# Performance work log

Hardware: AMD Instinct MI355X
Metric: run time of the kernel (lower is better)

The kernel has to match this reference:

```python
import jax, jax.numpy as jnp
import numpy as np

D_MODEL = 256
D_HID = 128
EPS = 1e-5
MASK_VALUE = -10000.0


def _layer_norm(x, scale, bias):
    mu = jnp.mean(x, axis=-1, keepdims=True)
    var = jnp.mean(jnp.square(x - mu), axis=-1, keepdims=True)
    return (x - mu) * jax.lax.rsqrt(var + EPS) * scale + bias


def setup_inputs() -> dict:
    key = jax.random.key(0)
    ks = jax.random.split(key, 8)
    B, S = 32, 1024
    std = 0.02
    return {
        "x": jax.random.normal(ks[0], (B, S, D_MODEL), dtype=jnp.float32),
        "ln1_scale": jnp.ones((D_MODEL,), jnp.float32),
        "ln1_bias": jnp.zeros((D_MODEL,), jnp.float32),
        "w_qkv": jax.random.normal(ks[1], (D_MODEL, 3 * D_MODEL), jnp.float32) * std,
        "b_qkv": jnp.zeros((3 * D_MODEL,), jnp.float32),
        "w_proj": jax.random.normal(ks[2], (D_MODEL, D_MODEL), jnp.float32) * std,
        "b_proj": jnp.zeros((D_MODEL,), jnp.float32),
        "ln2_scale": jnp.ones((D_MODEL,), jnp.float32),
        "ln2_bias": jnp.zeros((D_MODEL,), jnp.float32),
        "w_fc1": jax.random.normal(ks[3], (D_MODEL, D_HID), jnp.float32) * std,
        "b_fc1": jnp.zeros((D_HID,), jnp.float32),
        "w_fc2": jax.random.normal(ks[4], (D_HID, D_MODEL), jnp.float32) * std,
        "b_fc2": jnp.zeros((D_MODEL,), jnp.float32),
    }


def reference(x, ln1_scale, ln1_bias, w_qkv, b_qkv, w_proj, b_proj,
              ln2_scale, ln2_bias, w_fc1, b_fc1, w_fc2, b_fc2):
    B, S, D = x.shape
    # --- pre-LN self-attention ---
    residual = x
    h = _layer_norm(x, ln1_scale, ln1_bias)
    qkv = h @ w_qkv + b_qkv                       # [B, S, 3D]
    q, k, v = jnp.split(qkv, 3, axis=2)           # each [B, S, D]; 1 head, head_dim=D
    scale = 1.0 / jnp.sqrt(jnp.asarray(D, x.dtype))
    scores = jnp.einsum('bqd,bkd->bqk', q, k) * scale   # [B, S, S]
    causal = jnp.tril(jnp.ones((S, S), dtype=bool))
    scores = jnp.where(causal[None, :, :], scores, MASK_VALUE)
    attn = jax.nn.softmax(scores, axis=-1)        # dropout is identity (eval mode)
    out = jnp.einsum('bqk,bkd->bqd', attn, v)     # [B, S, D]
    out = out @ w_proj + b_proj
    x = out + residual
    # --- pre-LN MLP ---
    residual = x
    h = _layer_norm(x, ln2_scale, ln2_bias)
    h = jax.nn.relu(h @ w_fc1 + b_fc1)
    h = h @ w_fc2 + b_fc2
    return h + residual
```

## Files before the change

### kernel.cpp

```cpp
#include <hip/hip_runtime.h>
#include <hip/hip_bf16.h>

#define D_MODEL 256
#define D_HID   128
#define SEQ     1024
#define NBATCH  32
#define NROWS   (NBATCH * SEQ)
#define MASKV   -10000.0f
#define EPSLN   1e-5f

typedef unsigned short u16;
using bf16x8 = __attribute__((ext_vector_type(8))) short;
using f32x4  = __attribute__((ext_vector_type(4))) float;

union U8 { uint4 v; u16 s[8]; };

__device__ __forceinline__ float bf2f(u16 u) {
    unsigned int x = ((unsigned int)u) << 16;
    return __uint_as_float(x);
}
__device__ __forceinline__ u16 f2bf(float f) {
    unsigned int u = __float_as_uint(f);
    u += 0x7fff + ((u >> 16) & 1);
    return (u16)(u >> 16);
}
__device__ __forceinline__ void load4(const float* p, float* f) {
    float4 a = *(const float4*)p;
    f[0] = a.x; f[1] = a.y; f[2] = a.z; f[3] = a.w;
}
__device__ __forceinline__ void load4(const u16* p, float* f) {
    ushort4 v = *(const ushort4*)p;
    f[0] = bf2f(v.x); f[1] = bf2f(v.y); f[2] = bf2f(v.z); f[3] = bf2f(v.w);
}
__device__ __forceinline__ void gload16(const u16* g, u16* l) {
    __builtin_amdgcn_global_load_lds(
        (const __attribute__((address_space(1))) void*)g,
        (__attribute__((address_space(3))) void*)l, 16, 0, 0);
}

template <int CTRL>
__device__ __forceinline__ float dpp_mov(float v) {
    return __int_as_float(__builtin_amdgcn_update_dpp(
        0, __float_as_int(v), CTRL, 0xf, 0xf, true));
}
__device__ __forceinline__ float red16_max(float v) {
    v = fmaxf(v, dpp_mov<0xB1>(v));
    v = fmaxf(v, dpp_mov<0x4E>(v));
    v = fmaxf(v, dpp_mov<0x141>(v));
    v = fmaxf(v, dpp_mov<0x140>(v));
    return v;
}
__device__ __forceinline__ float red16_sum(float v) {
    v += dpp_mov<0xB1>(v);
    v += dpp_mov<0x4E>(v);
    v += dpp_mov<0x141>(v);
    v += dpp_mov<0x140>(v);
    return v;
}

__global__ __launch_bounds__(256) void transpose_weights(
    const float* __restrict__ wqkv, u16* __restrict__ wqkvT,
    const float* __restrict__ wproj, u16* __restrict__ wprojT,
    const float* __restrict__ wfc1, u16* __restrict__ wfc1T,
    const float* __restrict__ wfc2, u16* __restrict__ wfc2T) {
    int tid = blockIdx.x * 256 + threadIdx.x;
    int stride = gridDim.x * 256;
    for (int i = tid; i < 768 * 256; i += stride) {
        int n = i >> 8, k = i & 255;
        wqkvT[i] = f2bf(wqkv[k * 768 + n]);
    }
    for (int i = tid; i < 256 * 256; i += stride) {
        int n = i >> 8, k = i & 255;
        wprojT[i] = f2bf(wproj[k * 256 + n]);
    }
    for (int i = tid; i < 128 * 256; i += stride) {
        int n = i >> 8, k = i & 255;
        wfc1T[i] = f2bf(wfc1[k * 128 + n]);
    }
    for (int i = tid; i < 256 * 128; i += stride) {
        int n = i >> 7, k = i & 127;
        wfc2T[i] = f2bf(wfc2[k * 256 + n]);
    }
}

template <typename TX>
__global__ __launch_bounds__(256) void ln_fused(
    const TX* __restrict__ x, const float* __restrict__ gamma,
    const float* __restrict__ beta, u16* __restrict__ out) {
    int wave = threadIdx.x >> 6, lane = threadIdx.x & 63;
    int row = blockIdx.x * 4 + wave;
    float f[4];
    load4(x + (size_t)row * D_MODEL + lane * 4, f);
    float s  = f[0] + f[1] + f[2] + f[3];
    float sq = f[0] * f[0] + f[1] * f[1] + f[2] * f[2] + f[3] * f[3];
    #pragma unroll
    for (int off = 1; off < 64; off <<= 1) {
        s  += __shfl_xor(s, off);
        sq += __shfl_xor(sq, off);
    }
    float mu   = s * (1.0f / 256.0f);
    float var  = sq * (1.0f / 256.0f) - mu * mu;
    float rstd = rsqrtf(var + EPSLN);
    float g[4], be[4];
    load4(gamma + lane * 4, g);
    load4(beta + lane * 4, be);
    ushort4 o;
    o.x = f2bf((f[0] - mu) * rstd * g[0] + be[0]);
    o.y = f2bf((f[1] - mu) * rstd * g[1] + be[1]);
    o.z = f2bf((f[2] - mu) * rstd * g[2] + be[2]);
    o.w = f2bf((f[3] - mu) * rstd * g[3] + be[3]);
    *(ushort4*)(out + (size_t)row * D_MODEL + lane * 4) = o;
}

#define GEMM_LDS_ELEMS ((128 + 64) * 136)

template <int K>
__device__ __forceinline__ void gemm_tile(
    const u16* __restrict__ A, const u16* __restrict__ BT,
    int m0, int n0, u16* lds, f32x4 acc[4][2]) {
    constexpr int KC = 128, KP = 136;
    u16* ldsA = lds;
    u16* ldsB = lds + 128 * KP;
    const int tid = threadIdx.x;
    const int lane = tid & 63, wave = tid >> 6;
    const int wr = (wave >> 1) * 64, wc = (wave & 1) * 32;
    const int row = lane & 15, quad = lane >> 4;

    for (int ks = 0; ks < K; ks += KC) {
        __syncthreads();
        for (int i = tid; i < 2048; i += 256) {
            int i8 = i * 8;
            int r = i8 >> 7, c = i8 & 127;
            *(uint4*)(ldsA + r * KP + c) =
                *(const uint4*)(A + (size_t)(m0 + r) * K + ks + c);
        }
        for (int i = tid; i < 1024; i += 256) {
            int i8 = i * 8;
            int r = i8 >> 7, c = i8 & 127;
            *(uint4*)(ldsB + r * KP + c) =
                *(const uint4*)(BT + (size_t)(n0 + r) * K + ks + c);
        }
        __syncthreads();
        #pragma unroll
        for (int k0 = 0; k0 < KC; k0 += 32) {
            bf16x8 a[4], b[2];
            #pragma unroll
            for (int mi = 0; mi < 4; mi++)
                a[mi] = *(const bf16x8*)(ldsA + (wr + mi * 16 + row) * KP + k0 + quad * 8);
            #pragma unroll
            for (int nj = 0; nj < 2; nj++)
                b[nj] = *(const bf16x8*)(ldsB + (wc + nj * 16 + row) * KP + k0 + quad * 8);
            #pragma unroll
            for (int mi = 0; mi < 4; mi++)
                #pragma unroll
                for (int nj = 0; nj < 2; nj++)
                    acc[mi][nj] = __builtin_amdgcn_mfma_f32_16x16x32_bf16(
                        a[mi], b[nj], acc[mi][nj], 0, 0, 0);
        }
    }
}

#define ZERO_ACC(acc)                                        \
    _Pragma("unroll") for (int i_ = 0; i_ < 4; i_++)         \
    _Pragma("unroll") for (int j_ = 0; j_ < 2; j_++)         \
    _Pragma("unroll") for (int e_ = 0; e_ < 4; e_++) acc[i_][j_][e_] = 0.0f;

#define EPILOG_IDX                                           \
    int lane = threadIdx.x & 63, wave = threadIdx.x >> 6;    \
    int wr = (wave >> 1) * 64, wc = (wave & 1) * 32;         \
    int row = lane & 15, quad = lane >> 4;

__global__ __launch_bounds__(256) void gemm_qkv(
    const u16* __restrict__ h, const u16* __restrict__ wqkvT,
    const float* __restrict__ b_qkv,
    u16* __restrict__ q, u16* __restrict__ kk, u16* __restrict__ vT) {
    __shared__ u16 lds[GEMM_LDS_ELEMS];
    f32x4 acc[4][2];
    ZERO_ACC(acc)
    int m0 = blockIdx.x * 128, n0 = blockIdx.y * 64;
    gemm_tile<256>(h, wqkvT, m0, n0, lds, acc);
    EPILOG_IDX
    #pragma unroll
    for (int mi = 0; mi < 4; mi++) {
        #pragma unroll
        for (int nj = 0; nj < 2; nj++) {
            int gn = n0 + wc + nj * 16 + row;
            float bias = b_qkv[gn];
            int gm = m0 + wr + mi * 16 + quad * 4;
            if (gn < 256) {
                #pragma unroll
                for (int r = 0; r < 4; r++)
                    q[(size_t)(gm + r) * 256 + gn] =
                        f2bf((acc[mi][nj][r] + bias) * 0.0625f);
            } else if (gn < 512) {
                int col = gn - 256;
                #pragma unroll
                for (int r = 0; r < 4; r++)
                    kk[(size_t)(gm + r) * 256 + col] = f2bf(acc[mi][nj][r] + bias);
            } else {
                int d = gn - 512;
                int b = gm >> 10, s = gm & 1023;
                ushort4 pack;
                pack.x = f2bf(acc[mi][nj][0] + bias);
                pack.y = f2bf(acc[mi][nj][1] + bias);
                pack.z = f2bf(acc[mi][nj][2] + bias);
                pack.w = f2bf(acc[mi][nj][3] + bias);
                *(ushort4*)(vT + ((size_t)(b * 256 + d) << 10) + s) = pack;
            }
        }
    }
}

__global__ __launch_bounds__(256) void gemm_proj(
    const u16* __restrict__ ao, const u16* __restrict__ wprojT,
    const float* __restrict__ b_proj, const float* __restrict__ x_in,
    u16* __restrict__ x2) {
    __shared__ u16 lds[GEMM_LDS_ELEMS];
    f32x4 acc[4][2];
    ZERO_ACC(acc)
    int m0 = blockIdx.x * 128, n0 = blockIdx.y * 64;
    gemm_tile<256>(ao, wprojT, m0, n0, lds, acc);
    EPILOG_IDX
    #pragma unroll
    for (int mi = 0; mi < 4; mi++)
        #pragma unroll
        for (int nj = 0; nj < 2; nj++) {
            int gn = n0 + wc + nj * 16 + row;
            float bias = b_proj[gn];
            int gm = m0 + wr + mi * 16 + quad * 4;
            #pragma unroll
            for (int r = 0; r < 4; r++) {
                size_t idx = (size_t)(gm + r) * 256 + gn;
                x2[idx] = f2bf(acc[mi][nj][r] + bias + x_in[idx]);
            }
        }
}

__global__ __launch_bounds__(256) void gemm_fc1(
    const u16* __restrict__ h2, const u16* __restrict__ wfc1T,
    const float* __restrict__ b_fc1, u16* __restrict__ a1) {
    __shared__ u16 lds[GEMM_LDS_ELEMS];
    f32x4 acc[4][2];
    ZERO_ACC(acc)
    int m0 = blockIdx.x * 128, n0 = blockIdx.y * 64;
    gemm_tile<256>(h2, wfc1T, m0, n0, lds, acc);
    EPILOG_IDX
    #pragma unroll
    for (int mi = 0; mi < 4; mi++)
        #pragma unroll
        for (int nj = 0; nj < 2; nj++) {
            int gn = n0 + wc + nj * 16 + row;
            float bias = b_fc1[gn];
            int gm = m0 + wr + mi * 16 + quad * 4;
            #pragma unroll
            for (int r = 0; r < 4; r++) {
                float v = acc[mi][nj][r] + bias;
                a1[(size_t)(gm + r) * 128 + gn] = f2bf(fmaxf(v, 0.0f));
            }
        }
}

__global__ __launch_bounds__(256) void gemm_fc2(
    const u16* __restrict__ a1, const u16* __restrict__ wfc2T,
    const float* __restrict__ b_fc2, const u16* __restrict__ x2,
    float* __restrict__ out) {
    __shared__ u16 lds[GEMM_LDS_ELEMS];
    f32x4 acc[4][2];
    ZERO_ACC(acc)
    int m0 = blockIdx.x * 128, n0 = blockIdx.y * 64;
    gemm_tile<128>(a1, wfc2T, m0, n0, lds, acc);
    EPILOG_IDX
    #pragma unroll
    for (int mi = 0; mi < 4; mi++)
        #pragma unroll
        for (int nj = 0; nj < 2; nj++) {
            int gn = n0 + wc + nj * 16 + row;
            float bias = b_fc2[gn];
            int gm = m0 + wr + mi * 16 + quad * 4;
            #pragma unroll
            for (int r = 0; r < 4; r++) {
                size_t idx = (size_t)(gm + r) * 256 + gn;
                out[idx] = acc[mi][nj][r] + bias + bf2f(x2[idx]);
            }
        }
}

__constant__ unsigned char WQT[24] = {7,15,15,14,14,6,13,13,12,12,5,11,
                                      11,10,10,4,9,9,8,8,3,2,1,0};
__constant__ unsigned char WH[24]  = {2,0,1,0,1,2,0,1,0,1,2,0,
                                      1,0,1,2,0,1,0,1,2,2,2,2};

__global__ __launch_bounds__(256) void attn_kernel(
    const u16* __restrict__ q, const u16* __restrict__ k,
    const u16* __restrict__ vT, u16* __restrict__ ao,
    u16* __restrict__ part, float* __restrict__ ml) {
    __shared__ u16 k_lds[2][32 * 256];
    __shared__ u16 v_lds[2][256 * 32];
    __shared__ u16 p_lds[4][16 * 40];

    int j = blockIdx.x;
    int b = j & 31, w = j >> 5;
    int qt = WQT[w], hh = WH[w];
    int lo, hi;
    if (hh == 2) { lo = 0; hi = 2 * qt + 2; }
    else         { lo = hh * (qt + 1); hi = lo + qt + 1; }

    int tid = threadIdx.x;
    int lane = tid & 63, wave = tid >> 6;
    int row = lane & 15, quad = lane >> 4;
    int q0 = qt * 64;
    int qrow0 = q0 + wave * 16;

    const u16* qb = q + ((size_t)b << 10) * 256;
    const u16* kb = k + ((size_t)b << 10) * 256;
    const u16* vb = vT + (((size_t)b * 256) << 10);

    const int kxor = (row & 7) << 3;
    const int vxor = (row & 6) << 2;

    bf16x8 qf[8];
    #pragma unroll
    for (int kf = 0; kf < 8; kf++)
        qf[kf] = *(const bf16x8*)(qb + (size_t)(qrow0 + row) * 256 + kf * 32 + quad * 8);

    f32x4 o[16];
    #pragma unroll
    for (int n = 0; n < 16; n++)
        #pragma unroll
        for (int e = 0; e < 4; e++) o[n][e] = 0.0f;
    float m_i[4], l_i[4];
    #pragma unroll
    for (int r = 0; r < 4; r++) { m_i[r] = -1e30f; l_i[r] = 0.0f; }

    int wlast = 2 * qt + (wave >> 1);

    auto stage = [&](int bf, int kt) {
        int k0 = kt << 5;
        #pragma unroll
        for (int c = 0; c < 4; c++) {
            int blk = wave * 4 + c;
            int B = (blk << 10) + lane * 16;
            int rk = B >> 9;
            int ck = (B & 511) ^ ((rk & 7) << 4);
            gload16(kb + (size_t)(k0 + rk) * 256 + (ck >> 1),
                    &k_lds[bf][blk << 9]);
            int rv = B >> 6;
            int cv = (B & 63) ^ ((rv & 6) << 3);
            gload16(vb + ((size_t)rv << 10) + k0 + (cv >> 1),
                    &v_lds[bf][blk << 9]);
        }
    };

    stage(0, lo);
    __syncthreads();

    for (int kt = lo; kt < hi; kt++) {
        int cur = (kt - lo) & 1;
        if (kt + 1 < hi) stage(cur ^ 1, kt + 1);
        if (kt <= wlast) {
            const u16* kl = k_lds[cur];
            const u16* vl = v_lds[cur];

            f32x4 sf[2];
            #pragma unroll
            for (int jn = 0; jn < 2; jn++)
                #pragma unroll
                for (int e = 0; e < 4; e++) sf[jn][e] = 0.0f;
            __builtin_amdgcn_s_setprio(1);
            #pragma unroll
            for (int kf = 0; kf < 8; kf++)
                #pragma unroll
                for (int jn = 0; jn < 2; jn++) {
                    bf16x8 bfrag = *(const bf16x8*)(kl +
                        ((((jn * 16 + row) * 256) + kf * 32 + quad * 8) ^ kxor));
                    sf[jn] = __builtin_amdgcn_mfma_f32_16x16x32_bf16(
                        qf[kf], bfrag, sf[jn], 0, 0, 0);
                }
            __builtin_amdgcn_s_setprio(0);

            int kk0 = kt * 32;
            bool diag = (kt == wlast);
            int qrow = qrow0 + quad * 4;
            float sv[2][4];
            #pragma unroll
            for (int jn = 0; jn < 2; jn++)
                #pragma unroll
                for (int r = 0; r < 4; r++) {
                    float v = sf[jn][r];
                    if (diag && (kk0 + jn * 16 + row > qrow + r)) v = MASKV;
                    sv[jn][r] = v;
                }

            float pmax[4];
            int need = 0;
            #pragma unroll
            for (int r = 0; r < 4; r++) {
                pmax[r] = red16_max(fmaxf(sv[0][r], sv[1][r]));
                need |= (pmax[r] > m_i[r] + 8.0f) ? 1 : 0;
            }
            if (__any(need)) {
                #pragma unroll
                for (int r = 0; r < 4; r++) {
                    float mnew = fmaxf(m_i[r], pmax[r]);
                    float al = __expf(m_i[r] - mnew);
                    m_i[r] = mnew;
                    l_i[r] *= al;
                    #pragma unroll
                    for (int n = 0; n < 16; n++) o[n][r] *= al;
                }
            }
            #pragma unroll
            for (int r = 0; r < 4; r++) {
                float ps = 0.0f;
                #pragma unroll
                for (int jn = 0; jn < 2; jn++) {
                    sv[jn][r] = __expf(sv[jn][r] - m_i[r]);
                    ps += sv[jn][r];
                }
                l_i[r] += red16_sum(ps);
            }

            u16* pw = p_lds[wave];
            #pragma unroll
            for (int jn = 0; jn < 2; jn++)
                #pragma unroll
                for (int r = 0; r < 4; r++)
                    pw[(quad * 4 + r) * 40 + jn * 16 + row] = f2bf(sv[jn][r]);
            bf16x8 pf = *(const bf16x8*)(pw + row * 40 + quad * 8);

            __builtin_amdgcn_s_setprio(1);
            #pragma unroll
            for (int n = 0; n < 16; n++) {
                bf16x8 bv = *(const bf16x8*)(vl +
                    ((((n * 16 + row) * 32) + quad * 8) ^ vxor));
                o[n] = __builtin_amdgcn_mfma_f32_16x16x32_bf16(pf, bv, o[n], 0, 0, 0);
            }
            __builtin_amdgcn_s_setprio(0);
        }
        __syncthreads();
    }

    if (hh == 2) {
        float inv[4];
        #pragma unroll
        for (int r = 0; r < 4; r++) inv[r] = 1.0f / l_i[r];
        u16* aob = ao + (((size_t)b << 10) + qrow0) * 256;
        #pragma unroll
        for (int r = 0; r < 4; r++)
            #pragma unroll
            for (int n = 0; n < 16; n++)
                aob[(size_t)(quad * 4 + r) * 256 + n * 16 + row] =
                    f2bf(o[n][r] * inv[r]);
    } else {
        int p = (((b << 3) | (qt - 8)) << 1) | hh;
        u16* pb = part + (((size_t)p) << 6) * 256;
        #pragma unroll
        for (int r = 0; r < 4; r++) {
            int rt = wave * 16 + quad * 4 + r;
            #pragma unroll
            for (int n = 0; n < 16; n++)
                pb[(size_t)rt * 256 + n * 16 + row] = f2bf(o[n][r]);
        }
        if (row == 0) {
            #pragma unroll
            for (int r = 0; r < 4; r++) {
                int rt = wave * 16 + quad * 4 + r;
                float2 v2; v2.x = m_i[r]; v2.y = l_i[r];
                *(float2*)(ml + ((size_t)((p << 6) + rt)) * 2) = v2;
            }
        }
    }
}

__global__ __launch_bounds__(256) void attn_merge(
    const u16* __restrict__ part, const float* __restrict__ ml,
    u16* __restrict__ ao) {
    int j = blockIdx.x;
    int b = j >> 3, qi = j & 7;
    int t = threadIdx.x;
    int r = t >> 2, cq = t & 3;
    int pA = j << 1, pB = pA | 1;
    const float* mlA = ml + ((size_t)(pA << 6) + r) * 2;
    const float* mlB = ml + ((size_t)(pB << 6) + r) * 2;
    float mA = mlA[0], lA = mlA[1];
    float mB = mlB[0], lB = mlB[1];
    float m  = fmaxf(mA, mB);
    float eA = __expf(mA - m), eB = __expf(mB - m);
    float inv = 1.0f / (lA * eA + lB * eB);
    float sA = eA * inv, sB = eB * inv;
    const u16* oA = part + (((size_t)(pA << 6) + r) * 256) + cq * 64;
    const u16* oB = part + (((size_t)(pB << 6) + r) * 256) + cq * 64;
    u16* dst = ao + ((size_t)((b << 10) + 512 + (qi << 6) + r)) * 256 + cq * 64;
    #pragma unroll
    for (int u = 0; u < 8; u++) {
        U8 a, bb, o;
        a.v  = *(const uint4*)(oA + u * 8);
        bb.v = *(const uint4*)(oB + u * 8);
        #pragma unroll
        for (int e = 0; e < 8; e++)
            o.s[e] = f2bf(bf2f(a.s[e]) * sA + bf2f(bb.s[e]) * sB);
        *(uint4*)(dst + u * 8) = o.v;
    }
}

extern "C" void kernel_launch(void* const* d_in, const int* in_sizes, int n_in,
                              void* d_out, int out_size, void* d_ws, size_t ws_size,
                              hipStream_t stream) {
    const float* x      = (const float*)d_in[0];
    const float* ln1_s  = (const float*)d_in[1];
    const float* ln1_b  = (const float*)d_in[2];
    const float* w_qkv  = (const float*)d_in[3];
    const float* b_qkv  = (const float*)d_in[4];
    const float* w_proj = (const float*)d_in[5];
    const float* b_proj = (const float*)d_in[6];
    const float* ln2_s  = (const float*)d_in[7];
    const float* ln2_b  = (const float*)d_in[8];
    const float* w_fc1  = (const float*)d_in[9];
    const float* b_fc1  = (const float*)d_in[10];
    const float* w_fc2  = (const float*)d_in[11];
    const float* b_fc2  = (const float*)d_in[12];
    float* out = (float*)d_out;

    u16* h  = (u16*)d_out;
    u16* h2 = h + (size_t)NROWS * 256;

    u16* W = (u16*)d_ws;
    u16* wqkvT  = W;
    u16* wprojT = wqkvT + 196608;
    u16* wfc1T  = wprojT + 65536;
    u16* wfc2T  = wfc1T + 32768;
    u16* buf1   = wfc2T + 32768;
    u16* buf2   = buf1 + (size_t)NROWS * 256;
    u16* buf3   = buf2 + (size_t)NROWS * 256;

    u16*   part  = h;
    float* mlbuf = (float*)h2;

    transpose_weights<<<dim3(64), dim3(256), 0, stream>>>(
        w_qkv, wqkvT, w_proj, wprojT, w_fc1, wfc1T, w_fc2, wfc2T);
    ln_fused<float><<<dim3(NROWS / 4), dim3(256), 0, stream>>>(
        x, ln1_s, ln1_b, h);
    gemm_qkv<<<dim3(NROWS / 128, 12), dim3(256), 0, stream>>>(
        h, wqkvT, b_qkv, buf1, buf2, buf3);
    attn_kernel<<<dim3(768), dim3(256), 0, stream>>>(
        buf1, buf2, buf3, buf1, part, mlbuf);
    attn_merge<<<dim3(256), dim3(256), 0, stream>>>(
        part, mlbuf, buf1);
    gemm_proj<<<dim3(NROWS / 128, 4), dim3(256), 0, stream>>>(
        buf1, wprojT, b_proj, x, buf2);
    ln_fused<u16><<<dim3(NROWS / 4), dim3(256), 0, stream>>>(
        buf2, ln2_s, ln2_b, h2);
    gemm_fc1<<<dim3(NROWS / 128, 2), dim3(256), 0, stream>>>(
        h2, wfc1T, b_fc1, buf3);
    gemm_fc2<<<dim3(NROWS / 128, 4), dim3(256), 0, stream>>>(
        buf3, wfc2T, b_fc2, buf2, out);
}
```

Measured before the change: 274.9 us.

## Enlarge attention query tiles to 128 rows with new split-KV work schedule

Each attention wave now handles 32 query rows (two 16-row MFMA tiles), so each K/V fragment loaded from LDS is reused twice and the block covers 128 queries. The causal work is redistributed through new constant tables into 16 chunks per batch (512 blocks), with longer query tiles split into 2–4 KV ranges whose partials are stored transposed and merged by a generalized multi-chunk merge kernel. The goal is less LDS and global K/V traffic per FLOP and balanced load. The cost is doubled accumulator registers under launch_bounds(256,2), a more complex merge with strided column writes, and a partial buffer placed at a fixed offset in the output.

```diff
diff --git a/kernel.cpp b/kernel.cpp
--- a/kernel.cpp
+++ b/kernel.cpp
@@ -285,31 +285,27 @@
         }
 }
 
-__constant__ unsigned char WQT[24] = {7,15,15,14,14,6,13,13,12,12,5,11,
-                                      11,10,10,4,9,9,8,8,3,2,1,0};
-__constant__ unsigned char WH[24]  = {2,0,1,0,1,2,0,1,0,1,2,0,
-                                      1,0,1,2,0,1,0,1,2,2,2,2};
-
-__global__ __launch_bounds__(256) void attn_kernel(
+__constant__ unsigned char CQT[16] = {5,1,5,3,2,3,4,7,4,7,6,6,6,7,0,7};
+__constant__ unsigned char CLO[16] = {0,0,12,0,0,8,0,0,10,8,0,10,19,16,0,24};
+__constant__ unsigned char CHI[16] = {12,8,24,8,12,16,10,8,20,16,10,19,28,24,4,32};
+__constant__ unsigned char CPI[16] = {4,255,5,0,255,1,2,9,3,10,6,7,8,11,255,12};
+
+__global__ __launch_bounds__(256, 2) void attn_kernel(
     const u16* __restrict__ q, const u16* __restrict__ k,
     const u16* __restrict__ vT, u16* __restrict__ ao,
     u16* __restrict__ part, float* __restrict__ ml) {
     __shared__ u16 k_lds[2][32 * 256];
     __shared__ u16 v_lds[2][256 * 32];
-    __shared__ u16 p_lds[4][16 * 40];
+    __shared__ u16 p_lds[4][32 * 40];
 
     int j = blockIdx.x;
-    int b = j & 31, w = j >> 5;
-    int qt = WQT[w], hh = WH[w];
-    int lo, hi;
-    if (hh == 2) { lo = 0; hi = 2 * qt + 2; }
-    else         { lo = hh * (qt + 1); hi = lo + qt + 1; }
+    int b = j >> 4, c = j & 15;
+    int qt = CQT[c], lo = CLO[c], hi = CHI[c], pi = CPI[c];
 
     int tid = threadIdx.x;
     int lane = tid & 63, wave = tid >> 6;
     int row = lane & 15, quad = lane >> 4;
-    int q0 = qt * 64;
-    int qrow0 = q0 + wave * 16;
+    int qrowbase = qt * 128 + wave * 32;
 
     const u16* qb = q + ((size_t)b << 10) * 256;
     const u16* kb = k + ((size_t)b << 10) * 256;
@@ -318,27 +314,34 @@
     const int kxor = (row & 7) << 3;
     const int vxor = (row & 6) << 2;
 
-    bf16x8 qf[8];
-    #pragma unroll
-    for (int kf = 0; kf < 8; kf++)
-        qf[kf] = *(const bf16x8*)(qb + (size_t)(qrow0 + row) * 256 + kf * 32 + quad * 8);
-
-    f32x4 o[16];
-    #pragma unroll
-    for (int n = 0; n < 16; n++)
-        #pragma unroll
-        for (int e = 0; e < 4; e++) o[n][e] = 0.0f;
-    float m_i[4], l_i[4];
-    #pragma unroll
-    for (int r = 0; r < 4; r++) { m_i[r] = -1e30f; l_i[r] = 0.0f; }
-
-    int wlast = 2 * qt + (wave >> 1);
+    bf16x8 qf[2][8];
+    #pragma unroll
+    for (int mi = 0; mi < 2; mi++)
+        #pragma unroll
+        for (int kf = 0; kf < 8; kf++)
+            qf[mi][kf] = *(const bf16x8*)(qb +
+                (size_t)(qrowbase + mi * 16 + row) * 256 + kf * 32 + quad * 8);
+
+    f32x4 o[2][16];
+    #pragma unroll
+    for (int mi = 0; mi < 2; mi++)
+        #pragma unroll
+        for (int n = 0; n < 16; n++)
+            #pragma unroll
+            for (int e = 0; e < 4; e++) o[mi][n][e] = 0.0f;
+    float m_i[2][4], l_i[2][4];
+    #pragma unroll
+    for (int mi = 0; mi < 2; mi++)
+        #pragma unroll
+        for (int r = 0; r < 4; r++) { m_i[mi][r] = -1e30f; l_i[mi][r] = 0.0f; }
+
+    int wlast = 4 * qt + wave;
 
     auto stage = [&](int bf, int kt) {
         int k0 = kt << 5;
         #pragma unroll
-        for (int c = 0; c < 4; c++) {
-            int blk = wave * 4 + c;
+        for (int cc = 0; cc < 4; cc++) {
+            int blk = wave * 4 + cc;
             int B = (blk << 10) + lane * 16;
             int rk = B >> 9;
             int ck = (B & 511) ^ ((rk & 7) << 4);
@@ -361,11 +364,13 @@
             const u16* kl = k_lds[cur];
             const u16* vl = v_lds[cur];
 
-            f32x4 sf[2];
-            #pragma unroll
-            for (int jn = 0; jn < 2; jn++)
-                #pragma unroll
-                for (int e = 0; e < 4; e++) sf[jn][e] = 0.0f;
+            f32x4 sf[2][2];
+            #pragma unroll
+            for (int mi = 0; mi < 2; mi++)
+                #pragma unroll
+                for (int jn = 0; jn < 2; jn++)
+                    #pragma unroll
+                    for (int e = 0; e < 4; e++) sf[mi][jn][e] = 0.0f;
             __builtin_amdgcn_s_setprio(1);
             #pragma unroll
             for (int kf = 0; kf < 8; kf++)
@@ -373,133 +378,174 @@
                 for (int jn = 0; jn < 2; jn++) {
                     bf16x8 bfrag = *(const bf16x8*)(kl +
                         ((((jn * 16 + row) * 256) + kf * 32 + quad * 8) ^ kxor));
-                    sf[jn] = __builtin_amdgcn_mfma_f32_16x16x32_bf16(
-                        qf[kf], bfrag, sf[jn], 0, 0, 0);
+                    #pragma unroll
+                    for (int mi = 0; mi < 2; mi++)
+                        sf[mi][jn] = __builtin_amdgcn_mfma_f32_16x16x32_bf16(
+                            qf[mi][kf], bfrag, sf[mi][jn], 0, 0, 0);
                 }
             __builtin_amdgcn_s_setprio(0);
 
             int kk0 = kt * 32;
             bool diag = (kt == wlast);
-            int qrow = qrow0 + quad * 4;
-            float sv[2][4];
-            #pragma unroll
-            for (int jn = 0; jn < 2; jn++)
+            if (diag) {
+                #pragma unroll
+                for (int mi = 0; mi < 2; mi++)
+                    #pragma unroll
+                    for (int jn = 0; jn < 2; jn++)
+                        #pragma unroll
+                        for (int r = 0; r < 4; r++)
+                            if (kk0 + jn * 16 + row >
+                                qrowbase + mi * 16 + quad * 4 + r)
+                                sf[mi][jn][r] = MASKV;
+            }
+
+            float pmax[2][4];
+            int need = 0;
+            #pragma unroll
+            for (int mi = 0; mi < 2; mi++)
                 #pragma unroll
                 for (int r = 0; r < 4; r++) {
-                    float v = sf[jn][r];
-                    if (diag && (kk0 + jn * 16 + row > qrow + r)) v = MASKV;
-                    sv[jn][r] = v;
+                    pmax[mi][r] = red16_max(fmaxf(sf[mi][0][r], sf[mi][1][r]));
+                    need |= (pmax[mi][r] > m_i[mi][r] + 8.0f) ? 1 : 0;
                 }
-
-            float pmax[4];
-            int need = 0;
-            #pragma unroll
-            for (int r = 0; r < 4; r++) {
-                pmax[r] = red16_max(fmaxf(sv[0][r], sv[1][r]));
-                need |= (pmax[r] > m_i[r] + 8.0f) ? 1 : 0;
-            }
             if (__any(need)) {
                 #pragma unroll
+                for (int mi = 0; mi < 2; mi++)
+                    #pragma unroll
+                    for (int r = 0; r < 4; r++) {
+                        float mnew = fmaxf(m_i[mi][r], pmax[mi][r]);
+                        float al = __expf(m_i[mi][r] - mnew);
+                        m_i[mi][r] = mnew;
+                        l_i[mi][r] *= al;
+                        #pragma unroll
+                        for (int n = 0; n < 16; n++) o[mi][n][r] *= al;
+                    }
+            }
+            #pragma unroll
+            for (int mi = 0; mi < 2; mi++)
+                #pragma unroll
                 for (int r = 0; r < 4; r++) {
-                    float mnew = fmaxf(m_i[r], pmax[r]);
-                    float al = __expf(m_i[r] - mnew);
-                    m_i[r] = mnew;
-                    l_i[r] *= al;
+                    float ps = 0.0f;
                     #pragma unroll
-                    for (int n = 0; n < 16; n++) o[n][r] *= al;
+                    for (int jn = 0; jn < 2; jn++) {
+                        sf[mi][jn][r] = __expf(sf[mi][jn][r] - m_i[mi][r]);
+                        ps += sf[mi][jn][r];
+                    }
+                    l_i[mi][r] += red16_sum(ps);
                 }
-            }
-            #pragma unroll
-            for (int r = 0; r < 4; r++) {
-                float ps = 0.0f;
-                #pragma unroll
-                for (int jn = 0; jn < 2; jn++) {
-                    sv[jn][r] = __expf(sv[jn][r] - m_i[r]);
-                    ps += sv[jn][r];
-                }
-                l_i[r] += red16_sum(ps);
-            }
 
             u16* pw = p_lds[wave];
             #pragma unroll
-            for (int jn = 0; jn < 2; jn++)
-                #pragma unroll
-                for (int r = 0; r < 4; r++)
-                    pw[(quad * 4 + r) * 40 + jn * 16 + row] = f2bf(sv[jn][r]);
-            bf16x8 pf = *(const bf16x8*)(pw + row * 40 + quad * 8);
+            for (int mi = 0; mi < 2; mi++)
+                #pragma unroll
+                for (int jn = 0; jn < 2; jn++)
+                    #pragma unroll
+                    for (int r = 0; r < 4; r++)
+                        pw[(mi * 16 + quad * 4 + r) * 40 + jn * 16 + row] =
+                            f2bf(sf[mi][jn][r]);
+            bf16x8 pf0 = *(const bf16x8*)(pw + row * 40 + quad * 8);
+            bf16x8 pf1 = *(const bf16x8*)(pw + (16 + row) * 40 + quad * 8);
 
             __builtin_amdgcn_s_setprio(1);
             #pragma unroll
             for (int n = 0; n < 16; n++) {
                 bf16x8 bv = *(const bf16x8*)(vl +
                     ((((n * 16 + row) * 32) + quad * 8) ^ vxor));
-                o[n] = __builtin_amdgcn_mfma_f32_16x16x32_bf16(pf, bv, o[n], 0, 0, 0);
+                o[0][n] = __builtin_amdgcn_mfma_f32_16x16x32_bf16(pf0, bv, o[0][n], 0, 0, 0);
+                o[1][n] = __builtin_amdgcn_mfma_f32_16x16x32_bf16(pf1, bv, o[1][n], 0, 0, 0);
             }
             __builtin_amdgcn_s_setprio(0);
         }
         __syncthreads();
     }
 
-    if (hh == 2) {
-        float inv[4];
-        #pragma unroll
-        for (int r = 0; r < 4; r++) inv[r] = 1.0f / l_i[r];
-        u16* aob = ao + (((size_t)b << 10) + qrow0) * 256;
-        #pragma unroll
-        for (int r = 0; r < 4; r++)
-            #pragma unroll
-            for (int n = 0; n < 16; n++)
-                aob[(size_t)(quad * 4 + r) * 256 + n * 16 + row] =
-                    f2bf(o[n][r] * inv[r]);
+    if (pi == 255) {
+        u16* aob = ao + (((size_t)b << 10) + qrowbase) * 256;
+        #pragma unroll
+        for (int mi = 0; mi < 2; mi++)
+            #pragma unroll
+            for (int r = 0; r < 4; r++) {
+                float inv = 1.0f / l_i[mi][r];
+                #pragma unroll
+                for (int n = 0; n < 16; n++)
+                    aob[(size_t)(mi * 16 + quad * 4 + r) * 256 + n * 16 + row] =
+                        f2bf(o[mi][n][r] * inv);
+            }
     } else {
-        int p = (((b << 3) | (qt - 8)) << 1) | hh;
-        u16* pb = part + (((size_t)p) << 6) * 256;
-        #pragma unroll
-        for (int r = 0; r < 4; r++) {
-            int rt = wave * 16 + quad * 4 + r;
-            #pragma unroll
-            for (int n = 0; n < 16; n++)
-                pb[(size_t)rt * 256 + n * 16 + row] = f2bf(o[n][r]);
-        }
+        u16* pb = part + ((size_t)(b * 13 + pi) << 15);
+        int rbase = wave * 32 + quad * 4;
+        #pragma unroll
+        for (int mi = 0; mi < 2; mi++)
+            #pragma unroll
+            for (int n = 0; n < 16; n++) {
+                ushort4 pk;
+                pk.x = f2bf(o[mi][n][0]);
+                pk.y = f2bf(o[mi][n][1]);
+                pk.z = f2bf(o[mi][n][2]);
+                pk.w = f2bf(o[mi][n][3]);
+                *(ushort4*)(pb + (size_t)(n * 16 + row) * 128 + rbase + mi * 16) = pk;
+            }
         if (row == 0) {
             #pragma unroll
-            for (int r = 0; r < 4; r++) {
-                int rt = wave * 16 + quad * 4 + r;
-                float2 v2; v2.x = m_i[r]; v2.y = l_i[r];
-                *(float2*)(ml + ((size_t)((p << 6) + rt)) * 2) = v2;
-            }
-        }
-    }
-}
+            for (int mi = 0; mi < 2; mi++)
+                #pragma unroll
+                for (int r = 0; r < 4; r++) {
+                    int rt = wave * 32 + mi * 16 + quad * 4 + r;
+                    float2 v2; v2.x = m_i[mi][r]; v2.y = l_i[mi][r];
+                    *(float2*)(ml + ((size_t)((b * 13 + pi) * 128 + rt)) * 2) = v2;
+                }
+        }
+    }
+}
+
+__constant__ unsigned char SP_PB[5] = {0, 2, 4, 6, 9};
+__constant__ unsigned char SP_NC[5] = {2, 2, 2, 3, 4};
 
 __global__ __launch_bounds__(256) void attn_merge(
     const u16* __restrict__ part, const float* __restrict__ ml,
     u16* __restrict__ ao) {
+    __shared__ float s_sc[4][128];
     int j = blockIdx.x;
-    int b = j >> 3, qi = j & 7;
-    int t = threadIdx.x;
-    int r = t >> 2, cq = t & 3;
-    int pA = j << 1, pB = pA | 1;
-    const float* mlA = ml + ((size_t)(pA << 6) + r) * 2;
-    const float* mlB = ml + ((size_t)(pB << 6) + r) * 2;
-    float mA = mlA[0], lA = mlA[1];
-    float mB = mlB[0], lB = mlB[1];
-    float m  = fmaxf(mA, mB);
-    float eA = __expf(mA - m), eB = __expf(mB - m);
-    float inv = 1.0f / (lA * eA + lB * eB);
-    float sA = eA * inv, sB = eB * inv;
-    const u16* oA = part + (((size_t)(pA << 6) + r) * 256) + cq * 64;
-    const u16* oB = part + (((size_t)(pB << 6) + r) * 256) + cq * 64;
-    u16* dst = ao + ((size_t)((b << 10) + 512 + (qi << 6) + r)) * 256 + cq * 64;
-    #pragma unroll
-    for (int u = 0; u < 8; u++) {
-        U8 a, bb, o;
-        a.v  = *(const uint4*)(oA + u * 8);
-        bb.v = *(const uint4*)(oB + u * 8);
+    int b = j / 5, t = j - b * 5;
+    int pb0 = SP_PB[t], nc = SP_NC[t];
+    int tid = threadIdx.x;
+    if (tid < 128) {
+        int r = tid;
+        float mm[4], lv[4];
+        float mx = -1e30f;
+        for (int cc = 0; cc < nc; cc++) {
+            const float* p2 = ml + ((size_t)((b * 13 + pb0 + cc) * 128 + r)) * 2;
+            mm[cc] = p2[0]; lv[cc] = p2[1];
+            mx = fmaxf(mx, mm[cc]);
+        }
+        float lsum = 0.0f;
+        for (int cc = 0; cc < nc; cc++) {
+            mm[cc] = __expf(mm[cc] - mx);
+            lsum += lv[cc] * mm[cc];
+        }
+        float inv = 1.0f / lsum;
+        for (int cc = 0; cc < nc; cc++) s_sc[cc][r] = mm[cc] * inv;
+    }
+    __syncthreads();
+    int col = tid;
+    const u16* pc[4];
+    for (int cc = 0; cc < 4; cc++)
+        pc[cc] = part + ((size_t)(b * 13 + pb0 + (cc < nc ? cc : 0)) << 15)
+               + (size_t)col * 128;
+    u16* dst = ao + ((size_t)((b << 10) + (t + 3) * 128)) * 256 + col;
+    for (int u = 0; u < 16; u++) {
+        float acc[8];
+        #pragma unroll
+        for (int e = 0; e < 8; e++) acc[e] = 0.0f;
+        for (int cc = 0; cc < nc; cc++) {
+            U8 v; v.v = *(const uint4*)(pc[cc] + u * 8);
+            #pragma unroll
+            for (int e = 0; e < 8; e++)
+                acc[e] += s_sc[cc][u * 8 + e] * bf2f(v.s[e]);
+        }
         #pragma unroll
         for (int e = 0; e < 8; e++)
-            o.s[e] = f2bf(bf2f(a.s[e]) * sA + bf2f(bb.s[e]) * sB);
-        *(uint4*)(dst + u * 8) = o.v;
+            dst[(size_t)(u * 8 + e) * 256] = f2bf(acc[e]);
     }
 }
 
@@ -533,8 +579,8 @@
     u16* buf2   = buf1 + (size_t)NROWS * 256;
     u16* buf3   = buf2 + (size_t)NROWS * 256;
 
-    u16*   part  = h;
-    float* mlbuf = (float*)h2;
+    u16*   part  = (u16*)d_out;
+    float* mlbuf = (float*)d_out + 7200000;
 
     transpose_weights<<<dim3(64), dim3(256), 0, stream>>>(
         w_qkv, wqkvT, w_proj, wprojT, w_fc1, wfc1T, w_fc2, wfc2T);
@@ -542,9 +588,9 @@
         x, ln1_s, ln1_b, h);
     gemm_qkv<<<dim3(NROWS / 128, 12), dim3(256), 0, stream>>>(
         h, wqkvT, b_qkv, buf1, buf2, buf3);
-    attn_kernel<<<dim3(768), dim3(256), 0, stream>>>(
+    attn_kernel<<<dim3(512), dim3(256), 0, stream>>>(
         buf1, buf2, buf3, buf1, part, mlbuf);
-    attn_merge<<<dim3(256), dim3(256), 0, stream>>>(
+    attn_merge<<<dim3(160), dim3(256), 0, stream>>>(
         part, mlbuf, buf1);
     gemm_proj<<<dim3(NROWS / 128, 4), dim3(256), 0, stream>>>(
         buf1, wprojT, b_proj, x, buf2);
```

Measured after the change: 372.3 us. +35.4%, slower.

## Use 128x128 GEMM tiles with direct-to-LDS loads and XOR-swizzled layout

Applied to the files above, without the earlier changes.

The four dense GEMMs move from 128x64 output tiles to 128x128, so each wave computes a 64x64 sub-tile with 16 MFMA accumulators. Global-to-LDS staging now uses a gload16 helper (probably direct-to-LDS buffer loads) with an XOR swizzle on the column offset in place of row padding, and the LDS reads apply the same swizzle to avoid bank conflicts. The larger tiles raise arithmetic intensity and halve the grid sizes, at the cost of more registers per thread and fewer blocks to fill the GPU.

```diff
diff --git a/kernel.cpp b/kernel.cpp
--- a/kernel.cpp
+++ b/kernel.cpp
@@ -112,78 +112,82 @@
     *(ushort4*)(out + (size_t)row * D_MODEL + lane * 4) = o;
 }
 
-#define GEMM_LDS_ELEMS ((128 + 64) * 136)
+#define GT2_ELEMS (2 * 128 * 128)
 
 template <int K>
-__device__ __forceinline__ void gemm_tile(
+__device__ __forceinline__ void gemm_tile2(
     const u16* __restrict__ A, const u16* __restrict__ BT,
-    int m0, int n0, u16* lds, f32x4 acc[4][2]) {
-    constexpr int KC = 128, KP = 136;
+    int m0, int n0, u16* lds, f32x4 acc[4][4]) {
     u16* ldsA = lds;
-    u16* ldsB = lds + 128 * KP;
+    u16* ldsB = lds + 128 * 128;
     const int tid = threadIdx.x;
     const int lane = tid & 63, wave = tid >> 6;
-    const int wr = (wave >> 1) * 64, wc = (wave & 1) * 32;
+    const int wr = (wave >> 1) * 64, wc = (wave & 1) * 64;
     const int row = lane & 15, quad = lane >> 4;
 
-    for (int ks = 0; ks < K; ks += KC) {
+    for (int ks = 0; ks < K; ks += 128) {
         __syncthreads();
-        for (int i = tid; i < 2048; i += 256) {
-            int i8 = i * 8;
-            int r = i8 >> 7, c = i8 & 127;
-            *(uint4*)(ldsA + r * KP + c) =
-                *(const uint4*)(A + (size_t)(m0 + r) * K + ks + c);
-        }
-        for (int i = tid; i < 1024; i += 256) {
-            int i8 = i * 8;
-            int r = i8 >> 7, c = i8 & 127;
-            *(uint4*)(ldsB + r * KP + c) =
-                *(const uint4*)(BT + (size_t)(n0 + r) * K + ks + c);
+        #pragma unroll
+        for (int i = 0; i < 8; i++) {
+            int blk = i * 4 + wave;
+            int B = (blk << 10) + lane * 16;
+            int r = B >> 8;
+            int cb = (B & 255) ^ ((r & 7) << 4);
+            gload16(A + (size_t)(m0 + r) * K + ks + (cb >> 1),
+                    ldsA + (blk << 9));
+            gload16(BT + (size_t)(n0 + r) * K + ks + (cb >> 1),
+                    ldsB + (blk << 9));
         }
         __syncthreads();
         #pragma unroll
-        for (int k0 = 0; k0 < KC; k0 += 32) {
-            bf16x8 a[4], b[2];
+        for (int k0 = 0; k0 < 128; k0 += 32) {
+            bf16x8 a[4], b[4];
+            #pragma unroll
+            for (int mi = 0; mi < 4; mi++) {
+                int rr = wr + mi * 16 + row;
+                a[mi] = *(const bf16x8*)(ldsA + rr * 128 +
+                         ((k0 + quad * 8) ^ ((rr & 7) << 3)));
+            }
+            #pragma unroll
+            for (int nj = 0; nj < 4; nj++) {
+                int rr = wc + nj * 16 + row;
+                b[nj] = *(const bf16x8*)(ldsB + rr * 128 +
+                         ((k0 + quad * 8) ^ ((rr & 7) << 3)));
+            }
             #pragma unroll
             for (int mi = 0; mi < 4; mi++)
-                a[mi] = *(const bf16x8*)(ldsA + (wr + mi * 16 + row) * KP + k0 + quad * 8);
-            #pragma unroll
-            for (int nj = 0; nj < 2; nj++)
-                b[nj] = *(const bf16x8*)(ldsB + (wc + nj * 16 + row) * KP + k0 + quad * 8);
-            #pragma unroll
-            for (int mi = 0; mi < 4; mi++)
-                #pragma unroll
-                for (int nj = 0; nj < 2; nj++)
+                #pragma unroll
+                for (int nj = 0; nj < 4; nj++)
                     acc[mi][nj] = __builtin_amdgcn_mfma_f32_16x16x32_bf16(
                         a[mi], b[nj], acc[mi][nj], 0, 0, 0);
         }
     }
 }
 
-#define ZERO_ACC(acc)                                        \
+#define ZERO_ACC4(acc)                                       \
     _Pragma("unroll") for (int i_ = 0; i_ < 4; i_++)         \
-    _Pragma("unroll") for (int j_ = 0; j_ < 2; j_++)         \
+    _Pragma("unroll") for (int j_ = 0; j_ < 4; j_++)         \
     _Pragma("unroll") for (int e_ = 0; e_ < 4; e_++) acc[i_][j_][e_] = 0.0f;
 
-#define EPILOG_IDX                                           \
+#define EPILOG_IDX4                                          \
     int lane = threadIdx.x & 63, wave = threadIdx.x >> 6;    \
-    int wr = (wave >> 1) * 64, wc = (wave & 1) * 32;         \
+    int wr = (wave >> 1) * 64, wc = (wave & 1) * 64;         \
     int row = lane & 15, quad = lane >> 4;
 
 __global__ __launch_bounds__(256) void gemm_qkv(
     const u16* __restrict__ h, const u16* __restrict__ wqkvT,
     const float* __restrict__ b_qkv,
     u16* __restrict__ q, u16* __restrict__ kk, u16* __restrict__ vT) {
-    __shared__ u16 lds[GEMM_LDS_ELEMS];
-    f32x4 acc[4][2];
-    ZERO_ACC(acc)
-    int m0 = blockIdx.x * 128, n0 = blockIdx.y * 64;
-    gemm_tile<256>(h, wqkvT, m0, n0, lds, acc);
-    EPILOG_IDX
+    __shared__ u16 lds[GT2_ELEMS];
+    f32x4 acc[4][4];
+    ZERO_ACC4(acc)
+    int m0 = blockIdx.x * 128, n0 = blockIdx.y * 128;
+    gemm_tile2<256>(h, wqkvT, m0, n0, lds, acc);
+    EPILOG_IDX4
     #pragma unroll
     for (int mi = 0; mi < 4; mi++) {
         #pragma unroll
-        for (int nj = 0; nj < 2; nj++) {
+        for (int nj = 0; nj < 4; nj++) {
             int gn = n0 + wc + nj * 16 + row;
             float bias = b_qkv[gn];
             int gm = m0 + wr + mi * 16 + quad * 4;
@@ -215,16 +219,16 @@
     const u16* __restrict__ ao, const u16* __restrict__ wprojT,
     const float* __restrict__ b_proj, const float* __restrict__ x_in,
     u16* __restrict__ x2) {
-    __shared__ u16 lds[GEMM_LDS_ELEMS];
-    f32x4 acc[4][2];
-    ZERO_ACC(acc)
-    int m0 = blockIdx.x * 128, n0 = blockIdx.y * 64;
-    gemm_tile<256>(ao, wprojT, m0, n0, lds, acc);
-    EPILOG_IDX
+    __shared__ u16 lds[GT2_ELEMS];
+    f32x4 acc[4][4];
+    ZERO_ACC4(acc)
+    int m0 = blockIdx.x * 128, n0 = blockIdx.y * 128;
+    gemm_tile2<256>(ao, wprojT, m0, n0, lds, acc);
+    EPILOG_IDX4
     #pragma unroll
     for (int mi = 0; mi < 4; mi++)
         #pragma unroll
-        for (int nj = 0; nj < 2; nj++) {
+        for (int nj = 0; nj < 4; nj++) {
             int gn = n0 + wc + nj * 16 + row;
             float bias = b_proj[gn];
             int gm = m0 + wr + mi * 16 + quad * 4;
@@ -239,17 +243,17 @@
 __global__ __launch_bounds__(256) void gemm_fc1(
     const u16* __restrict__ h2, const u16* __restrict__ wfc1T,
     const float* __restrict__ b_fc1, u16* __restrict__ a1) {
-    __shared__ u16 lds[GEMM_LDS_ELEMS];
-    f32x4 acc[4][2];
-    ZERO_ACC(acc)
-    int m0 = blockIdx.x * 128, n0 = blockIdx.y * 64;
-    gemm_tile<256>(h2, wfc1T, m0, n0, lds, acc);
-    EPILOG_IDX
+    __shared__ u16 lds[GT2_ELEMS];
+    f32x4 acc[4][4];
+    ZERO_ACC4(acc)
+    int m0 = blockIdx.x * 128, n0 = 0;
+    gemm_tile2<256>(h2, wfc1T, m0, n0, lds, acc);
+    EPILOG_IDX4
     #pragma unroll
     for (int mi = 0; mi < 4; mi++)
         #pragma unroll
-        for (int nj = 0; nj < 2; nj++) {
-            int gn = n0 + wc + nj * 16 + row;
+        for (int nj = 0; nj < 4; nj++) {
+            int gn = wc + nj * 16 + row;
             float bias = b_fc1[gn];
             int gm = m0 + wr + mi * 16 + quad * 4;
             #pragma unroll
@@ -264,16 +268,16 @@
     const u16* __restrict__ a1, const u16* __restrict__ wfc2T,
     const float* __restrict__ b_fc2, const u16* __restrict__ x2,
     float* __restrict__ out) {
-    __shared__ u16 lds[GEMM_LDS_ELEMS];
-    f32x4 acc[4][2];
-    ZERO_ACC(acc)
-    int m0 = blockIdx.x * 128, n0 = blockIdx.y * 64;
-    gemm_tile<128>(a1, wfc2T, m0, n0, lds, acc);
-    EPILOG_IDX
+    __shared__ u16 lds[GT2_ELEMS];
+    f32x4 acc[4][4];
+    ZERO_ACC4(acc)
+    int m0 = blockIdx.x * 128, n0 = blockIdx.y * 128;
+    gemm_tile2<128>(a1, wfc2T, m0, n0, lds, acc);
+    EPILOG_IDX4
     #pragma unroll
     for (int mi = 0; mi < 4; mi++)
         #pragma unroll
-        for (int nj = 0; nj < 2; nj++) {
+        for (int nj = 0; nj < 4; nj++) {
             int gn = n0 + wc + nj * 16 + row;
             float bias = b_fc2[gn];
             int gm = m0 + wr + mi * 16 + quad * 4;
@@ -540,18 +544,18 @@
         w_qkv, wqkvT, w_proj, wprojT, w_fc1, wfc1T, w_fc2, wfc2T);
     ln_fused<float><<<dim3(NROWS / 4), dim3(256), 0, stream>>>(
         x, ln1_s, ln1_b, h);
-    gemm_qkv<<<dim3(NROWS / 128, 12), dim3(256), 0, stream>>>(
+    gemm_qkv<<<dim3(NROWS / 128, 6), dim3(256), 0, stream>>>(
         h, wqkvT, b_qkv, buf1, buf2, buf3);
     attn_kernel<<<dim3(768), dim3(256), 0, stream>>>(
         buf1, buf2, buf3, buf1, part, mlbuf);
     attn_merge<<<dim3(256), dim3(256), 0, stream>>>(
         part, mlbuf, buf1);
-    gemm_proj<<<dim3(NROWS / 128, 4), dim3(256), 0, stream>>>(
+    gemm_proj<<<dim3(NROWS / 128, 2), dim3(256), 0, stream>>>(
         buf1, wprojT, b_proj, x, buf2);
     ln_fused<u16><<<dim3(NROWS / 4), dim3(256), 0, stream>>>(
         buf2, ln2_s, ln2_b, h2);
-    gemm_fc1<<<dim3(NROWS / 128, 2), dim3(256), 0, stream>>>(
+    gemm_fc1<<<dim3(NROWS / 128, 1), dim3(256), 0, stream>>>(
         h2, wfc1T, b_fc1, buf3);
-    gemm_fc2<<<dim3(NROWS / 128, 4), dim3(256), 0, stream>>>(
+    gemm_fc2<<<dim3(NROWS / 128, 2), dim3(256), 0, stream>>>(
         buf3, wfc2T, b_fc2, buf2, out);
 }
```

New measurement: 251.7 us. 8.4% less time.
